# Performance work log

Measured on AMD Instinct MI355X. Metric: run time of the kernel, lower is better.

Reference implementation:

```python
import jax, jax.numpy as jnp
import numpy as np

H = 256          # hidden_channels
R = 64           # num_rbf
N = 20000        # nodes
E = 320000       # edges
CUTOFF_LO = 0.0
CUTOFF_UP = 5.0
LN_EPS = 1e-5


def _layernorm(x, g, b):
    mu = jnp.mean(x, axis=-1, keepdims=True)
    var = jnp.var(x, axis=-1, keepdims=True)
    return (x - mu) * jax.lax.rsqrt(var + LN_EPS) * g + b


def _cosine_cutoff(r):
    # cutoff_lower == 0 branch of CosineCutoff
    c = 0.5 * (jnp.cos(r * (jnp.pi / CUTOFF_UP)) + 1.0)
    return c * (r < CUTOFF_UP).astype(r.dtype)


def setup_inputs() -> dict:
    key = jax.random.key(0)
    ks = jax.random.split(key, 16)
    def xavier(k, shape):
        fan_in, fan_out = shape[1], shape[0]
        lim = np.sqrt(6.0 / (fan_in + fan_out))
        return jax.random.uniform(k, shape, jnp.float32, -lim, lim)
    x = jax.random.normal(ks[0], (N, H), jnp.float32)
    edge_index = jax.random.randint(ks[1], (2, E), 0, N, jnp.int64)
    edge_weight = jax.random.uniform(ks[2], (E,), jnp.float32, 0.0, CUTOFF_UP)
    edge_attr = jax.random.normal(ks[3], (E, R), jnp.float32)
    return {
        "x": x,
        "edge_index": edge_index,
        "edge_weight": edge_weight,
        "edge_attr": edge_attr,
        "ln_g": jnp.ones((H,), jnp.float32),
        "ln_b": jnp.zeros((H,), jnp.float32),
        "Wq": xavier(ks[4], (H, H)), "bq": jnp.zeros((H,), jnp.float32),
        "Wk": xavier(ks[5], (H, H)), "bk": jnp.zeros((H,), jnp.float32),
        "Wv": xavier(ks[6], (H, H)), "bv": jnp.zeros((H,), jnp.float32),
        "Wo": xavier(ks[7], (H, H)), "bo": jnp.zeros((H,), jnp.float32),
        "Wdk": xavier(ks[8], (H, R)), "bdk": jnp.zeros((H,), jnp.float32),
        "Wdv": xavier(ks[9], (H, R)), "bdv": jnp.zeros((H,), jnp.float32),
    }


def reference(x, edge_index, edge_weight, edge_attr,
              ln_g, ln_b, Wq, bq, Wk, bk, Wv, bv, Wo, bo, Wdk, bdk, Wdv, bdv):
    src = edge_index[0]  # j (messages come from)
    dst = edge_index[1]  # i (messages aggregate to)

    x_norm = _layernorm(x, ln_g, ln_b)                     # [N,H]
    q = x_norm @ Wq.T + bq                                 # [N,H]
    k = x_norm @ Wk.T + bk
    v = x_norm @ Wv.T + bv

    dk = jax.nn.silu(edge_attr @ Wdk.T + bdk)              # [E,H]
    dv = jax.nn.silu(edge_attr @ Wdv.T + bdv)              # [E,H]

    q_i = q[dst]                                           # [E,H]
    k_j = k[src]
    v_j = v[src]

    attn = jnp.sum(q_i * k_j * dk, axis=1)                 # [E]
    attn = jax.nn.silu(attn) * _cosine_cutoff(edge_weight) # [E]

    msg = v_j * dv * attn[:, None]                         # [E,H]
    agg = jax.ops.segment_sum(msg, dst, num_segments=x.shape[0])  # [N,H]

    out = agg @ Wo.T + bo
    return x + out
```

## Files before the change

### kernel.cpp

```cpp
#include <hip/hip_runtime.h>
#include <math.h>

#define NN 20000
#define H 256
#define R 64
#define EE 320000
#define LN_EPS 1e-5f
#define NB 79

using short8  = __attribute__((ext_vector_type(8))) short;
using ushort8 = __attribute__((ext_vector_type(8))) unsigned short;
using f32x4   = __attribute__((ext_vector_type(4))) float;

__device__ __forceinline__ float silu_f(float x) {
    return x * __builtin_amdgcn_rcpf(1.0f + __expf(-x));
}

__device__ __forceinline__ unsigned short f2bf(float f) {
    unsigned u = __float_as_uint(f);
    u += 0x7fff + ((u >> 16) & 1);
    return (unsigned short)(u >> 16);
}
__device__ __forceinline__ float bf2f(unsigned short s) {
    return __uint_as_float(((unsigned)s) << 16);
}
__device__ __forceinline__ unsigned short f2h(float f) {
    unsigned r;
    asm("v_cvt_f16_f32 %0, %1" : "=v"(r) : "v"(f));
    return (unsigned short)r;
}
__device__ __forceinline__ float h2f(unsigned short h) {
    float f;
    asm("v_cvt_f32_f16 %0, %1" : "=v"(f) : "v"((unsigned)h));
    return f;
}

__device__ __forceinline__ int dh_idx(int row, int col) {
    return row * 256 + (col ^ (((row >> 2) & 3) << 4));
}

__global__ __launch_bounds__(256) void k_prep(
    const float* __restrict__ Wq, const float* __restrict__ Wk,
    const float* __restrict__ Wv, const float* __restrict__ Wo,
    const float* __restrict__ g,  const float* __restrict__ b,
    const float* __restrict__ bq, const float* __restrict__ bk, const float* __restrict__ bv,
    const float* __restrict__ Wdk, const float* __restrict__ Wdv,
    unsigned short* __restrict__ wqkv_p, unsigned short* __restrict__ wo_p,
    unsigned short* __restrict__ wdk_p,  unsigned short* __restrict__ wdv_p,
    float* __restrict__ bias3, int* __restrict__ hist)
{
    const int bid = blockIdx.x, t = threadIdx.x;
    if (bid < 128) {
        const int mat = bid >> 5;
        const float* W = mat == 0 ? Wq : (mat == 1 ? Wk : (mat == 2 ? Wv : Wo));
        unsigned short* out = (mat < 3) ? wqkv_p + (size_t)mat * 131072 : wo_p;
        const int fold = mat < 3;
        const int flat = (bid & 31) * 256 + t;
        const int tile = flat >> 9;
        const int rem  = flat & 511;
        const int ks   = rem >> 6;
        const int lane = rem & 63;
        const int nl = lane & 15, quad = lane >> 4;
        const int h  = tile * 16 + nl;
        const int c0 = ks * 32 + quad * 8;
        short8 hi8, lo8;
        #pragma unroll
        for (int j = 0; j < 8; ++j) {
            float wv = W[(size_t)h * 256 + c0 + j];
            if (fold) wv *= g[c0 + j];
            const unsigned short hh = f2bf(wv);
            hi8[j] = (short)hh;
            lo8[j] = (short)f2bf(wv - bf2f(hh));
        }
        unsigned short* ob = out + ((size_t)(tile * 8 + ks)) * 1024;
        *(short8*)&ob[lane * 8] = hi8;
        *(short8*)&ob[512 + lane * 8] = lo8;
    } else if (bid < 144) {
        const int flat = (bid - 128) * 256 + t;
        const int mat  = flat >> 11;
        const int rem  = flat & 2047;
        const int hh   = rem >> 10;
        const int r2   = rem & 1023;
        const int tile = r2 >> 7;
        const int r3   = r2 & 127;
        const int ks   = r3 >> 6;
        const int lane = r3 & 63;
        const int nl = lane & 15, quad = lane >> 4;
        const float* W = mat == 0 ? Wdk : Wdv;
        unsigned short* out = (mat == 0 ? wdk_p : wdv_p)
                            + hh * 16384 + (tile * 2 + ks) * 1024 + lane * 8;
        const float* wr = W + (size_t)(hh * 128 + tile * 16 + nl) * 64 + ks * 32 + quad * 8;
        const float4 w0 = *(const float4*)wr;
        const float4 w1 = *(const float4*)(wr + 4);
        const float zz[8] = {w0.x, w0.y, w0.z, w0.w, w1.x, w1.y, w1.z, w1.w};
        short8 hi8, lo8;
        #pragma unroll
        for (int j = 0; j < 8; ++j) {
            const unsigned short hv = f2bf(zz[j]);
            hi8[j] = (short)hv;
            lo8[j] = (short)f2bf(zz[j] - bf2f(hv));
        }
        *(short8*)out = hi8;
        *(short8*)(out + 512) = lo8;
    } else if (bid < 147) {
        const int mat = bid - 144, h = t;
        const float* W  = mat == 0 ? Wq : (mat == 1 ? Wk : Wv);
        const float* bb = mat == 0 ? bq : (mat == 1 ? bk : bv);
        float s = 0.f;
        const float* wr = W + (size_t)h * 256;
        for (int c = 0; c < 256; c += 4) {
            const float4 w4 = *(const float4*)(wr + c);
            const float4 b4 = *(const float4*)(b + c);
            s += w4.x * b4.x + w4.y * b4.y + w4.z * b4.z + w4.w * b4.w;
        }
        bias3[mat * 256 + h] = bb[h] + s;
    } else {
        const int i = (bid - 147) * 256 + t;
        if (i < NN) hist[i] = 0;
    }
}

__global__ __launch_bounds__(64, 2) void k_ln_qkv(
    const float* __restrict__ x,
    const unsigned short* __restrict__ wqkv_p, const float* __restrict__ bias3,
    unsigned short* __restrict__ q, unsigned short* __restrict__ k,
    unsigned short* __restrict__ v)
{
    const int t = threadIdx.x;
    const int lane = t & 63;
    const int nl = lane & 15, quad = lane >> 4;
    const int nbase = blockIdx.x * 16;
    const int node = nbase + nl;
    const bool nv = node < NN;

    float xv[64];
    float sum = 0.f, sq = 0.f;
    {
        const float* xp = x + (size_t)node * H + quad * 8;
        #pragma unroll
        for (int ks = 0; ks < 8; ++ks) {
            float4 x0 = {0.f,0.f,0.f,0.f}, x1 = {0.f,0.f,0.f,0.f};
            if (nv) {
                x0 = *(const float4*)(xp + ks * 32);
                x1 = *(const float4*)(xp + ks * 32 + 4);
            }
            xv[ks*8+0]=x0.x; xv[ks*8+1]=x0.y; xv[ks*8+2]=x0.z; xv[ks*8+3]=x0.w;
            xv[ks*8+4]=x1.x; xv[ks*8+5]=x1.y; xv[ks*8+6]=x1.z; xv[ks*8+7]=x1.w;
            sum += x0.x+x0.y+x0.z+x0.w + x1.x+x1.y+x1.z+x1.w;
            sq  += x0.x*x0.x+x0.y*x0.y+x0.z*x0.z+x0.w*x0.w
                 + x1.x*x1.x+x1.y*x1.y+x1.z*x1.z+x1.w*x1.w;
        }
    }
    sum += __shfl_xor(sum, 16); sum += __shfl_xor(sum, 32);
    sq  += __shfl_xor(sq, 16);  sq  += __shfl_xor(sq, 32);
    const float mu  = sum * (1.0f / H);
    const float var = sq * (1.0f / H) - mu * mu;
    const float rs  = rsqrtf(var + LN_EPS);

    short8 a_hi[8], a_lo[8];
    #pragma unroll
    for (int ks = 0; ks < 8; ++ks) {
        #pragma unroll
        for (int j = 0; j < 8; ++j) {
            const float z = (xv[ks*8+j] - mu) * rs;
            const unsigned short hh = f2bf(z);
            a_hi[ks][j] = (short)hh;
            a_lo[ks][j] = (short)f2bf(z - bf2f(hh));
        }
    }

    for (int mat = 0; mat < 3; ++mat) {
        unsigned short* outp = mat == 0 ? q : (mat == 1 ? k : v);
        const float* bp = bias3 + mat * 256;
        const unsigned short* wb = wqkv_p + (size_t)mat * 131072 + lane * 8;
        for (int tile = 0; tile < 16; ++tile) {
            const unsigned short* gb = wb + (size_t)tile * 8192;
            const float bbv = bp[tile * 16 + nl];
            f32x4 acc = {bbv, bbv, bbv, bbv};
            #pragma unroll
            for (int ks = 0; ks < 8; ++ks) {
                const short8 b_hi = *(const short8*)(gb + ks * 1024);
                const short8 b_lo = *(const short8*)(gb + ks * 1024 + 512);
                acc = __builtin_amdgcn_mfma_f32_16x16x32_bf16(a_hi[ks], b_hi, acc, 0, 0, 0);
                acc = __builtin_amdgcn_mfma_f32_16x16x32_bf16(a_lo[ks], b_hi, acc, 0, 0, 0);
                acc = __builtin_amdgcn_mfma_f32_16x16x32_bf16(a_hi[ks], b_lo, acc, 0, 0, 0);
            }
            #pragma unroll
            for (int r = 0; r < 4; ++r) {
                const int onode = nbase + quad * 4 + r;
                if (onode < NN)
                    outp[(size_t)onode * H + tile * 16 + nl] = f2h(acc[r]);
            }
        }
    }
}

__global__ __launch_bounds__(256) void k_hist(const int* __restrict__ ei, int* __restrict__ hist) {
    int e = blockIdx.x * 256 + threadIdx.x;
    if (e < EE) atomicAdd(&hist[ei[EE + e]], 1);
}

__global__ __launch_bounds__(256) void k_scan1(const int* __restrict__ hist,
                                               int* __restrict__ cursor, int* __restrict__ bsum) {
    const int t = threadIdx.x, i = blockIdx.x * 256 + t;
    const int lane = t & 63, w = t >> 6;
    const int v = (i < NN) ? hist[i] : 0;
    int incl = v;
    #pragma unroll
    for (int off = 1; off < 64; off <<= 1) {
        int u = __shfl_up(incl, off);
        if (lane >= off) incl += u;
    }
    __shared__ int ws[4];
    if (lane == 63) ws[w] = incl;
    __syncthreads();
    int base = 0;
    #pragma unroll
    for (int j = 0; j < 4; ++j) if (j < w) base += ws[j];
    if (i < NN) cursor[i] = base + incl - v;
    if (t == 255) bsum[blockIdx.x] = base + incl;
}

__global__ __launch_bounds__(128) void k_scan2(int* __restrict__ bsum) {
    __shared__ int buf[128];
    const int t = threadIdx.x;
    const int v = (t < NB) ? bsum[t] : 0;
    buf[t] = v;
    __syncthreads();
    #pragma unroll
    for (int off = 1; off < 128; off <<= 1) {
        int add = (t >= off) ? buf[t - off] : 0;
        __syncthreads();
        buf[t] += add;
        __syncthreads();
    }
    if (t < NB) bsum[t] = buf[t] - v;
}

__global__ __launch_bounds__(256) void k_scatter(const int* __restrict__ ei,
                                                 const float* __restrict__ ew,
                                                 int* __restrict__ cursor,
                                                 const int* __restrict__ bsum,
                                                 int* __restrict__ perm,
                                                 int* __restrict__ srcs,
                                                 int* __restrict__ dsts,
                                                 float* __restrict__ ews) {
    int e = blockIdx.x * 256 + threadIdx.x;
    if (e < EE) {
        int s = ei[e];
        int d = ei[EE + e];
        int pos = atomicAdd(&cursor[d], 1) + bsum[d >> 8];
        perm[pos] = e;
        srcs[pos] = s;
        dsts[pos] = d;
        ews[pos] = ew[e];
    }
}

__global__ __launch_bounds__(256, 4) void k_edge(
    const unsigned short* __restrict__ q16, const unsigned short* __restrict__ k16,
    const unsigned short* __restrict__ v16,
    const float* __restrict__ ea,
    const unsigned short* __restrict__ wdk_p, const float* __restrict__ bdk,
    const unsigned short* __restrict__ wdv_p, const float* __restrict__ bdv,
    const int* __restrict__ perm, const int* __restrict__ srcs,
    const int* __restrict__ dsts, const float* __restrict__ ews,
    float* __restrict__ agg)
{
    __shared__ __align__(16) unsigned short dks_all[4 * 16 * 256];
    __shared__ int   srcw_all[4 * 16], dstw_all[4 * 16];
    __shared__ float attw_all[4 * 16];

    const int t    = threadIdx.x;
    const int bi   = blockIdx.x;
    const int wave = t >> 6, lane = t & 63;
    const int eb2  = (((bi & 7) * 625 + (bi >> 3)) * 4 + wave) * 16;

    unsigned short* dksw = dks_all + wave * 4096;
    int*   srcw = srcw_all + wave * 16;
    int*   dstw = dstw_all + wave * 16;
    float* attw = attw_all + wave * 16;

    const int nl = lane & 15, quad = lane >> 4;
    const int tx = lane & 31, ty2 = lane >> 5;
    const int h0 = tx * 4, e0l = ty2 * 8;

    if (lane < 16) {
        srcw[lane] = srcs[eb2 + lane];
        dstw[lane] = dsts[eb2 + lane];
    }

    short8 a_hi[2], a_lo[2];
    {
        const int e = perm[eb2 + nl];
        const float* ap = ea + (size_t)e * R + quad * 8;
        #pragma unroll
        for (int ks = 0; ks < 2; ++ks) {
            const f32x4 x0 = *(const f32x4*)(ap + ks * 32);
            const f32x4 x1 = *(const f32x4*)(ap + ks * 32 + 4);
            const float zz[8] = {x0[0], x0[1], x0[2], x0[3], x1[0], x1[1], x1[2], x1[3]};
            #pragma unroll
            for (int j = 0; j < 8; ++j) {
                const unsigned short hv = f2bf(zz[j]);
                a_hi[ks][j] = (short)hv;
                a_lo[ks][j] = (short)f2bf(zz[j] - bf2f(hv));
            }
        }
    }

    #define MFMA_DKS(IMG, BIAS, HALF)                                                 \
    {                                                                                 \
        const unsigned short* img_ = (IMG);                                           \
        f32x4 accA[8];                                                                \
        _Pragma("unroll")                                                             \
        for (int tt = 0; tt < 8; ++tt) {                                              \
            short8 b_hi[2], b_lo[2];                                                  \
            _Pragma("unroll")                                                         \
            for (int ks = 0; ks < 2; ++ks) {                                          \
                const unsigned short* fb = img_ + (tt * 2 + ks) * 1024 + lane * 8;    \
                b_hi[ks] = *(const short8*)fb;                                        \
                b_lo[ks] = *(const short8*)(fb + 512);                                \
            }                                                                         \
            const float bb = (BIAS)[(HALF) * 128 + tt * 16 + nl];                     \
            f32x4 acc = {bb, bb, bb, bb};                                             \
            _Pragma("unroll")                                                         \
            for (int ks = 0; ks < 2; ++ks) {                                          \
                acc = __builtin_amdgcn_mfma_f32_16x16x32_bf16(a_hi[ks], b_hi[ks], acc, 0, 0, 0); \
                acc = __builtin_amdgcn_mfma_f32_16x16x32_bf16(a_lo[ks], b_hi[ks], acc, 0, 0, 0); \
                acc = __builtin_amdgcn_mfma_f32_16x16x32_bf16(a_hi[ks], b_lo[ks], acc, 0, 0, 0); \
            }                                                                         \
            accA[tt] = acc;                                                           \
        }                                                                             \
        _Pragma("unroll")                                                             \
        for (int tt = 0; tt < 8; ++tt)                                                \
            _Pragma("unroll")                                                         \
            for (int r = 0; r < 4; ++r)                                               \
                dksw[dh_idx(quad * 4 + r, (HALF) * 128 + tt * 16 + nl)] =             \
                    f2h(silu_f(accA[tt][r]));                                         \
    }

    MFMA_DKS(wdk_p,         bdk, 0);
    MFMA_DKS(wdk_p + 16384, bdk, 1);

    {
        float qv[8];
        int pd = -1;
        #pragma unroll
        for (int i = 0; i < 8; ++i) {
            const int d = dstw[e0l + i], s = srcw[e0l + i];
            if (d != pd) {
                const ushort4 q0 = *(const ushort4*)(q16 + (size_t)d * H + h0);
                const ushort4 q1 = *(const ushort4*)(q16 + (size_t)d * H + 128 + h0);
                qv[0] = h2f(q0.x); qv[1] = h2f(q0.y); qv[2] = h2f(q0.z); qv[3] = h2f(q0.w);
                qv[4] = h2f(q1.x); qv[5] = h2f(q1.y); qv[6] = h2f(q1.z); qv[7] = h2f(q1.w);
                pd = d;
            }
            const ushort4 k0 = *(const ushort4*)(k16 + (size_t)s * H + h0);
            const ushort4 k1 = *(const ushort4*)(k16 + (size_t)s * H + 128 + h0);
            const ushort4 d40 = *(const ushort4*)&dksw[dh_idx(e0l + i, h0)];
            const ushort4 d41 = *(const ushort4*)&dksw[dh_idx(e0l + i, 128 + h0)];
            float part = qv[0] * h2f(k0.x) * h2f(d40.x) + qv[1] * h2f(k0.y) * h2f(d40.y)
                       + qv[2] * h2f(k0.z) * h2f(d40.z) + qv[3] * h2f(k0.w) * h2f(d40.w)
                       + qv[4] * h2f(k1.x) * h2f(d41.x) + qv[5] * h2f(k1.y) * h2f(d41.y)
                       + qv[6] * h2f(k1.z) * h2f(d41.z) + qv[7] * h2f(k1.w) * h2f(d41.w);
            #pragma unroll
            for (int off = 16; off; off >>= 1) part += __shfl_xor(part, off);
            if (tx == 0) attw[e0l + i] = part;
        }
    }

    if (lane < 16) {
        const float rr = ews[eb2 + lane];
        const float cut = (rr < 5.0f) ? 0.5f * (__cosf(rr * 0.6283185307f) + 1.0f) : 0.0f;
        attw[lane] = silu_f(attw[lane]) * cut;
    }

    MFMA_DKS(wdv_p,         bdv, 0);
    MFMA_DKS(wdv_p + 16384, bdv, 1);

    {
        float4 m0 = {0.f,0.f,0.f,0.f}, m1 = {0.f,0.f,0.f,0.f};
        int cur_d = -1;
        #pragma unroll
        for (int i = 0; i < 8; ++i) {
            const int d = dstw[e0l + i], s = srcw[e0l + i];
            const float a = attw[e0l + i];
            const ushort4 v0 = *(const ushort4*)(v16 + (size_t)s * H + h0);
            const ushort4 v1 = *(const ushort4*)(v16 + (size_t)s * H + 128 + h0);
            const ushort4 d40 = *(const ushort4*)&dksw[dh_idx(e0l + i, h0)];
            const ushort4 d41 = *(const ushort4*)&dksw[dh_idx(e0l + i, 128 + h0)];
            const float w0x = h2f(v0.x) * h2f(d40.x) * a, w0y = h2f(v0.y) * h2f(d40.y) * a;
            const float w0z = h2f(v0.z) * h2f(d40.z) * a, w0w = h2f(v0.w) * h2f(d40.w) * a;
            const float w1x = h2f(v1.x) * h2f(d41.x) * a, w1y = h2f(v1.y) * h2f(d41.y) * a;
            const float w1z = h2f(v1.z) * h2f(d41.z) * a, w1w = h2f(v1.w) * h2f(d41.w) * a;
            if (d != cur_d) {
                if (cur_d >= 0) {
                    float* dp = agg + (size_t)cur_d * H;
                    atomicAdd(dp + h0 + 0, m0.x); atomicAdd(dp + h0 + 1, m0.y);
                    atomicAdd(dp + h0 + 2, m0.z); atomicAdd(dp + h0 + 3, m0.w);
                    atomicAdd(dp + 128 + h0 + 0, m1.x); atomicAdd(dp + 128 + h0 + 1, m1.y);
                    atomicAdd(dp + 128 + h0 + 2, m1.z); atomicAdd(dp + 128 + h0 + 3, m1.w);
                }
                m0.x = w0x; m0.y = w0y; m0.z = w0z; m0.w = w0w;
                m1.x = w1x; m1.y = w1y; m1.z = w1z; m1.w = w1w;
                cur_d = d;
            } else {
                m0.x += w0x; m0.y += w0y; m0.z += w0z; m0.w += w0w;
                m1.x += w1x; m1.y += w1y; m1.z += w1z; m1.w += w1w;
            }
        }
        {
            float* dp = agg + (size_t)cur_d * H;
            atomicAdd(dp + h0 + 0, m0.x); atomicAdd(dp + h0 + 1, m0.y);
            atomicAdd(dp + h0 + 2, m0.z); atomicAdd(dp + h0 + 3, m0.w);
            atomicAdd(dp + 128 + h0 + 0, m1.x); atomicAdd(dp + 128 + h0 + 1, m1.y);
            atomicAdd(dp + 128 + h0 + 2, m1.z); atomicAdd(dp + 128 + h0 + 3, m1.w);
        }
    }
    #undef MFMA_DKS
}

__global__ __launch_bounds__(64, 2) void k_out(
    const float* __restrict__ aggm, const unsigned short* __restrict__ wo_p,
    const float* __restrict__ bo, const float* __restrict__ x, float* __restrict__ out)
{
    const int t = threadIdx.x;
    const int lane = t & 63;
    const int nl = lane & 15, quad = lane >> 4;
    const int nbase = blockIdx.x * 16;
    const int node = nbase + nl;
    const bool nv = node < NN;

    short8 a_hi[8], a_lo[8];
    {
        const float* ap = aggm + (size_t)node * H + quad * 8;
        #pragma unroll
        for (int ks = 0; ks < 8; ++ks) {
            float4 x0 = {0.f,0.f,0.f,0.f}, x1 = {0.f,0.f,0.f,0.f};
            if (nv) { x0 = *(const float4*)(ap + ks * 32); x1 = *(const float4*)(ap + ks * 32 + 4); }
            const float zz[8] = {x0.x,x0.y,x0.z,x0.w,x1.x,x1.y,x1.z,x1.w};
            #pragma unroll
            for (int j = 0; j < 8; ++j) {
                const unsigned short hh = f2bf(zz[j]);
                a_hi[ks][j] = (short)hh;
                a_lo[ks][j] = (short)f2bf(zz[j] - bf2f(hh));
            }
        }
    }
    for (int tile = 0; tile < 16; ++tile) {
        const unsigned short* gb = wo_p + (size_t)tile * 8192 + lane * 8;
        const float bbv = bo[tile * 16 + nl];
        f32x4 acc = {bbv, bbv, bbv, bbv};
        #pragma unroll
        for (int ks = 0; ks < 8; ++ks) {
            const short8 b_hi = *(const short8*)(gb + ks * 1024);
            const short8 b_lo = *(const short8*)(gb + ks * 1024 + 512);
            acc = __builtin_amdgcn_mfma_f32_16x16x32_bf16(a_hi[ks], b_hi, acc, 0, 0, 0);
            acc = __builtin_amdgcn_mfma_f32_16x16x32_bf16(a_lo[ks], b_hi, acc, 0, 0, 0);
            acc = __builtin_amdgcn_mfma_f32_16x16x32_bf16(a_hi[ks], b_lo, acc, 0, 0, 0);
        }
        #pragma unroll
        for (int r = 0; r < 4; ++r) {
            const int onode = nbase + quad * 4 + r;
            if (onode < NN) {
                const size_t oi = (size_t)onode * H + tile * 16 + nl;
                out[oi] = x[oi] + acc[r];
            }
        }
    }
}

extern "C" void kernel_launch(void* const* d_in, const int* in_sizes, int n_in,
                              void* d_out, int out_size, void* d_ws, size_t ws_size,
                              hipStream_t stream) {
    const float* x   = (const float*)d_in[0];
    const int*   ei  = (const int*)d_in[1];
    const float* ew  = (const float*)d_in[2];
    const float* ea  = (const float*)d_in[3];
    const float* g   = (const float*)d_in[4];
    const float* b   = (const float*)d_in[5];
    const float* Wq  = (const float*)d_in[6];  const float* bq  = (const float*)d_in[7];
    const float* Wk  = (const float*)d_in[8];  const float* bk  = (const float*)d_in[9];
    const float* Wv  = (const float*)d_in[10]; const float* bv  = (const float*)d_in[11];
    const float* Wo  = (const float*)d_in[12]; const float* bo  = (const float*)d_in[13];
    const float* Wdk = (const float*)d_in[14]; const float* bdk = (const float*)d_in[15];
    const float* Wdv = (const float*)d_in[16]; const float* bdv = (const float*)d_in[17];

    unsigned short* q16 = (unsigned short*)d_ws;
    unsigned short* k16 = q16 + (size_t)NN * H;
    unsigned short* v16 = k16 + (size_t)NN * H;
    float* agg  = (float*)(v16 + (size_t)NN * H);
    int*   hist = (int*)(agg + (size_t)NN * H);
    int*   cur  = hist + NN;
    int*   bsum = cur + NN;
    int*   perm = bsum + 128;
    int*   srcs = perm + EE;
    int*   dsts = srcs + EE;
    float* ews  = (float*)(dsts + EE);
    unsigned short* wqkv_p = (unsigned short*)(ews + EE);
    unsigned short* wo_p   = wqkv_p + 393216;
    unsigned short* wdk_p  = wo_p + 131072;
    unsigned short* wdv_p  = wdk_p + 32768;
    float* bias3 = (float*)(wdv_p + 32768);

    hipMemsetAsync(agg, 0, (size_t)NN * H * sizeof(float), stream);
    k_prep<<<226, 256, 0, stream>>>(Wq, Wk, Wv, Wo, g, b, bq, bk, bv, Wdk, Wdv,
                                    wqkv_p, wo_p, wdk_p, wdv_p, bias3, hist);
    k_hist<<<EE / 256, 256, 0, stream>>>(ei, hist);
    k_ln_qkv<<<(NN + 15) / 16, 64, 0, stream>>>(x, wqkv_p, bias3, q16, k16, v16);
    k_scan1<<<NB, 256, 0, stream>>>(hist, cur, bsum);
    k_scan2<<<1, 128, 0, stream>>>(bsum);
    k_scatter<<<EE / 256, 256, 0, stream>>>(ei, ew, cur, bsum, perm, srcs, dsts, ews);
    k_edge<<<EE / 64, 256, 0, stream>>>(q16, k16, v16, ea, wdk_p, bdk, wdv_p, bdv,
                                        perm, srcs, dsts, ews, agg);
    k_out<<<(NN + 15) / 16, 64, 0, stream>>>(agg, wo_p, bo, x, (float*)d_out);
}
```

Measured before the change: 628.0 us.

## Use fp16 MFMA for edge dk/dv projections with LDS-staged weights and persistent blocks

```diff
diff --git a/kernel.cpp b/kernel.cpp
--- a/kernel.cpp
+++ b/kernel.cpp
@@ -7,10 +7,16 @@
 #define EE 320000
 #define LN_EPS 1e-5f
 #define NB 79
+#define GEDGE 1000
 
 using short8  = __attribute__((ext_vector_type(8))) short;
 using ushort8 = __attribute__((ext_vector_type(8))) unsigned short;
 using f32x4   = __attribute__((ext_vector_type(4))) float;
+using half8   = __attribute__((ext_vector_type(8))) _Float16;
+using half2v  = __attribute__((ext_vector_type(2))) _Float16;
+
+typedef __attribute__((address_space(3))) unsigned int lds_uint;
+typedef const __attribute__((address_space(1))) unsigned int glb_uint;
 
 __device__ __forceinline__ float silu_f(float x) {
     return x * __builtin_amdgcn_rcpf(1.0f + __expf(-x));
@@ -88,20 +94,15 @@
         const int nl = lane & 15, quad = lane >> 4;
         const float* W = mat == 0 ? Wdk : Wdv;
         unsigned short* out = (mat == 0 ? wdk_p : wdv_p)
-                            + hh * 16384 + (tile * 2 + ks) * 1024 + lane * 8;
+                            + hh * 8192 + (tile * 2 + ks) * 512 + lane * 8;
         const float* wr = W + (size_t)(hh * 128 + tile * 16 + nl) * 64 + ks * 32 + quad * 8;
         const float4 w0 = *(const float4*)wr;
         const float4 w1 = *(const float4*)(wr + 4);
         const float zz[8] = {w0.x, w0.y, w0.z, w0.w, w1.x, w1.y, w1.z, w1.w};
-        short8 hi8, lo8;
-        #pragma unroll
-        for (int j = 0; j < 8; ++j) {
-            const unsigned short hv = f2bf(zz[j]);
-            hi8[j] = (short)hv;
-            lo8[j] = (short)f2bf(zz[j] - bf2f(hv));
-        }
-        *(short8*)out = hi8;
-        *(short8*)(out + 512) = lo8;
+        ushort8 p8;
+        #pragma unroll
+        for (int j = 0; j < 8; ++j) p8[j] = f2h(zz[j]);
+        *(ushort8*)out = p8;
     } else if (bid < 147) {
         const int mat = bid - 144, h = t;
         const float* W  = mat == 0 ? Wq : (mat == 1 ? Wk : Wv);
@@ -257,78 +258,50 @@
     }
 }
 
-__global__ __launch_bounds__(256, 4) void k_edge(
+__global__ __launch_bounds__(256, 1) void k_edge(
     const unsigned short* __restrict__ q16, const unsigned short* __restrict__ k16,
     const unsigned short* __restrict__ v16,
     const float* __restrict__ ea,
-    const unsigned short* __restrict__ wdk_p, const float* __restrict__ bdk,
-    const unsigned short* __restrict__ wdv_p, const float* __restrict__ bdv,
+    const unsigned short* __restrict__ wdkv_p,
+    const float* __restrict__ bdk, const float* __restrict__ bdv,
     const int* __restrict__ perm, const int* __restrict__ srcs,
     const int* __restrict__ dsts, const float* __restrict__ ews,
     float* __restrict__ agg)
 {
+    __shared__ __align__(16) unsigned short wlds[4 * 8192];
     __shared__ __align__(16) unsigned short dks_all[4 * 16 * 256];
-    __shared__ int   srcw_all[4 * 16], dstw_all[4 * 16];
-    __shared__ float attw_all[4 * 16];
 
     const int t    = threadIdx.x;
     const int bi   = blockIdx.x;
     const int wave = t >> 6, lane = t & 63;
-    const int eb2  = (((bi & 7) * 625 + (bi >> 3)) * 4 + wave) * 16;
-
-    unsigned short* dksw = dks_all + wave * 4096;
-    int*   srcw = srcw_all + wave * 16;
-    int*   dstw = dstw_all + wave * 16;
-    float* attw = attw_all + wave * 16;
-
     const int nl = lane & 15, quad = lane >> 4;
     const int tx = lane & 31, ty2 = lane >> 5;
     const int h0 = tx * 4, e0l = ty2 * 8;
 
-    if (lane < 16) {
-        srcw[lane] = srcs[eb2 + lane];
-        dstw[lane] = dsts[eb2 + lane];
-    }
-
-    short8 a_hi[2], a_lo[2];
+    unsigned short* dksw = dks_all + wave * 4096;
+
     {
-        const int e = perm[eb2 + nl];
-        const float* ap = ea + (size_t)e * R + quad * 8;
-        #pragma unroll
-        for (int ks = 0; ks < 2; ++ks) {
-            const f32x4 x0 = *(const f32x4*)(ap + ks * 32);
-            const f32x4 x1 = *(const f32x4*)(ap + ks * 32 + 4);
-            const float zz[8] = {x0[0], x0[1], x0[2], x0[3], x1[0], x1[1], x1[2], x1[3]};
-            #pragma unroll
-            for (int j = 0; j < 8; ++j) {
-                const unsigned short hv = f2bf(zz[j]);
-                a_hi[ks][j] = (short)hv;
-                a_lo[ks][j] = (short)f2bf(zz[j] - bf2f(hv));
-            }
-        }
-    }
-
-    #define MFMA_DKS(IMG, BIAS, HALF)                                                 \
+        const ushort8* sp = (const ushort8*)wdkv_p + t;
+        ushort8* dpw = (ushort8*)wlds + (t & 192);
+        #pragma unroll
+        for (int c = 0; c < 16; ++c)
+            __builtin_amdgcn_global_load_lds((glb_uint*)(sp + c * 256),
+                                             (lds_uint*)(dpw + c * 256), 16, 0, 0);
+    }
+    __syncthreads();
+
+    #define MFMA_DKS16(IMG, BIAS, HALF)                                               \
     {                                                                                 \
-        const unsigned short* img_ = (IMG);                                           \
+        const unsigned short* ib_ = wlds + (IMG) * 8192;                              \
         f32x4 accA[8];                                                                \
         _Pragma("unroll")                                                             \
         for (int tt = 0; tt < 8; ++tt) {                                              \
-            short8 b_hi[2], b_lo[2];                                                  \
-            _Pragma("unroll")                                                         \
-            for (int ks = 0; ks < 2; ++ks) {                                          \
-                const unsigned short* fb = img_ + (tt * 2 + ks) * 1024 + lane * 8;    \
-                b_hi[ks] = *(const short8*)fb;                                        \
-                b_lo[ks] = *(const short8*)(fb + 512);                                \
-            }                                                                         \
+            const half8 b0 = *(const half8*)&ib_[(tt * 2 + 0) * 512 + lane * 8];      \
+            const half8 b1 = *(const half8*)&ib_[(tt * 2 + 1) * 512 + lane * 8];      \
             const float bb = (BIAS)[(HALF) * 128 + tt * 16 + nl];                     \
             f32x4 acc = {bb, bb, bb, bb};                                             \
-            _Pragma("unroll")                                                         \
-            for (int ks = 0; ks < 2; ++ks) {                                          \
-                acc = __builtin_amdgcn_mfma_f32_16x16x32_bf16(a_hi[ks], b_hi[ks], acc, 0, 0, 0); \
-                acc = __builtin_amdgcn_mfma_f32_16x16x32_bf16(a_lo[ks], b_hi[ks], acc, 0, 0, 0); \
-                acc = __builtin_amdgcn_mfma_f32_16x16x32_bf16(a_hi[ks], b_lo[ks], acc, 0, 0, 0); \
-            }                                                                         \
+            acc = __builtin_amdgcn_mfma_f32_16x16x32_f16(af0, b0, acc, 0, 0, 0);      \
+            acc = __builtin_amdgcn_mfma_f32_16x16x32_f16(af1, b1, acc, 0, 0, 0);      \
             accA[tt] = acc;                                                           \
         }                                                                             \
         _Pragma("unroll")                                                             \
@@ -339,85 +312,127 @@
                     f2h(silu_f(accA[tt][r]));                                         \
     }
 
-    MFMA_DKS(wdk_p,         bdk, 0);
-    MFMA_DKS(wdk_p + 16384, bdk, 1);
-
-    {
-        float qv[8];
-        int pd = -1;
+    for (int it = 0; it < 5; ++it) {
+        const int chunk = (bi & 7) * 625 + (bi >> 3) * 5 + it;
+        const int eb2   = (chunk * 4 + wave) * 16;
+
+        half8 af0, af1;
+        {
+            const int e = perm[eb2 + nl];
+            const float* ap = ea + (size_t)e * R + quad * 8;
+            const f32x4 x0 = *(const f32x4*)(ap);
+            const f32x4 x1 = *(const f32x4*)(ap + 4);
+            const f32x4 x2 = *(const f32x4*)(ap + 32);
+            const f32x4 x3 = *(const f32x4*)(ap + 36);
+            #pragma unroll
+            for (int j = 0; j < 4; ++j) {
+                af0[j]     = (_Float16)x0[j];
+                af0[j + 4] = (_Float16)x1[j];
+                af1[j]     = (_Float16)x2[j];
+                af1[j + 4] = (_Float16)x3[j];
+            }
+        }
+
+        MFMA_DKS16(0, bdk, 0);
+        MFMA_DKS16(1, bdk, 1);
+
+        int srcr[8], dstr[8];
         #pragma unroll
         for (int i = 0; i < 8; ++i) {
-            const int d = dstw[e0l + i], s = srcw[e0l + i];
-            if (d != pd) {
-                const ushort4 q0 = *(const ushort4*)(q16 + (size_t)d * H + h0);
-                const ushort4 q1 = *(const ushort4*)(q16 + (size_t)d * H + 128 + h0);
-                qv[0] = h2f(q0.x); qv[1] = h2f(q0.y); qv[2] = h2f(q0.z); qv[3] = h2f(q0.w);
-                qv[4] = h2f(q1.x); qv[5] = h2f(q1.y); qv[6] = h2f(q1.z); qv[7] = h2f(q1.w);
-                pd = d;
-            }
-            const ushort4 k0 = *(const ushort4*)(k16 + (size_t)s * H + h0);
-            const ushort4 k1 = *(const ushort4*)(k16 + (size_t)s * H + 128 + h0);
-            const ushort4 d40 = *(const ushort4*)&dksw[dh_idx(e0l + i, h0)];
-            const ushort4 d41 = *(const ushort4*)&dksw[dh_idx(e0l + i, 128 + h0)];
-            float part = qv[0] * h2f(k0.x) * h2f(d40.x) + qv[1] * h2f(k0.y) * h2f(d40.y)
-                       + qv[2] * h2f(k0.z) * h2f(d40.z) + qv[3] * h2f(k0.w) * h2f(d40.w)
-                       + qv[4] * h2f(k1.x) * h2f(d41.x) + qv[5] * h2f(k1.y) * h2f(d41.y)
-                       + qv[6] * h2f(k1.z) * h2f(d41.z) + qv[7] * h2f(k1.w) * h2f(d41.w);
+            srcr[i] = srcs[eb2 + e0l + i];
+            dstr[i] = dsts[eb2 + e0l + i];
+        }
+
+        float att[8];
+        {
+            half2v qa, qb, qc, qd;
+            int pd = -1;
             #pragma unroll
-            for (int off = 16; off; off >>= 1) part += __shfl_xor(part, off);
-            if (tx == 0) attw[e0l + i] = part;
-        }
-    }
-
-    if (lane < 16) {
-        const float rr = ews[eb2 + lane];
-        const float cut = (rr < 5.0f) ? 0.5f * (__cosf(rr * 0.6283185307f) + 1.0f) : 0.0f;
-        attw[lane] = silu_f(attw[lane]) * cut;
-    }
-
-    MFMA_DKS(wdv_p,         bdv, 0);
-    MFMA_DKS(wdv_p + 16384, bdv, 1);
-
-    {
-        float4 m0 = {0.f,0.f,0.f,0.f}, m1 = {0.f,0.f,0.f,0.f};
-        int cur_d = -1;
+            for (int i = 0; i < 8; ++i) {
+                const int d = dstr[i], s = srcr[i];
+                if (d != pd) {
+                    const uint2 qq0 = *(const uint2*)(q16 + (size_t)d * H + h0);
+                    const uint2 qq1 = *(const uint2*)(q16 + (size_t)d * H + 128 + h0);
+                    qa = __builtin_bit_cast(half2v, qq0.x);
+                    qb = __builtin_bit_cast(half2v, qq0.y);
+                    qc = __builtin_bit_cast(half2v, qq1.x);
+                    qd = __builtin_bit_cast(half2v, qq1.y);
+                    pd = d;
+                }
+                const uint2 kk0 = *(const uint2*)(k16 + (size_t)s * H + h0);
+                const uint2 kk1 = *(const uint2*)(k16 + (size_t)s * H + 128 + h0);
+                const uint2 dd0 = *(const uint2*)&dksw[dh_idx(e0l + i, h0)];
+                const uint2 dd1 = *(const uint2*)&dksw[dh_idx(e0l + i, 128 + h0)];
+                float part = 0.f;
+                part = __builtin_amdgcn_fdot2(qa * __builtin_bit_cast(half2v, kk0.x),
+                                              __builtin_bit_cast(half2v, dd0.x), part, false);
+                part = __builtin_amdgcn_fdot2(qb * __builtin_bit_cast(half2v, kk0.y),
+                                              __builtin_bit_cast(half2v, dd0.y), part, false);
+                part = __builtin_amdgcn_fdot2(qc * __builtin_bit_cast(half2v, kk1.x),
+                                              __builtin_bit_cast(half2v, dd1.x), part, false);
+                part = __builtin_amdgcn_fdot2(qd * __builtin_bit_cast(half2v, kk1.y),
+                                              __builtin_bit_cast(half2v, dd1.y), part, false);
+                #pragma unroll
+                for (int off = 16; off; off >>= 1) part += __shfl_xor(part, off);
+                att[i] = part;
+            }
+        }
+
         #pragma unroll
         for (int i = 0; i < 8; ++i) {
-            const int d = dstw[e0l + i], s = srcw[e0l + i];
-            const float a = attw[e0l + i];
-            const ushort4 v0 = *(const ushort4*)(v16 + (size_t)s * H + h0);
-            const ushort4 v1 = *(const ushort4*)(v16 + (size_t)s * H + 128 + h0);
-            const ushort4 d40 = *(const ushort4*)&dksw[dh_idx(e0l + i, h0)];
-            const ushort4 d41 = *(const ushort4*)&dksw[dh_idx(e0l + i, 128 + h0)];
-            const float w0x = h2f(v0.x) * h2f(d40.x) * a, w0y = h2f(v0.y) * h2f(d40.y) * a;
-            const float w0z = h2f(v0.z) * h2f(d40.z) * a, w0w = h2f(v0.w) * h2f(d40.w) * a;
-            const float w1x = h2f(v1.x) * h2f(d41.x) * a, w1y = h2f(v1.y) * h2f(d41.y) * a;
-            const float w1z = h2f(v1.z) * h2f(d41.z) * a, w1w = h2f(v1.w) * h2f(d41.w) * a;
-            if (d != cur_d) {
-                if (cur_d >= 0) {
-                    float* dp = agg + (size_t)cur_d * H;
-                    atomicAdd(dp + h0 + 0, m0.x); atomicAdd(dp + h0 + 1, m0.y);
-                    atomicAdd(dp + h0 + 2, m0.z); atomicAdd(dp + h0 + 3, m0.w);
-                    atomicAdd(dp + 128 + h0 + 0, m1.x); atomicAdd(dp + 128 + h0 + 1, m1.y);
-                    atomicAdd(dp + 128 + h0 + 2, m1.z); atomicAdd(dp + 128 + h0 + 3, m1.w);
+            const float rr = ews[eb2 + e0l + i];
+            const float cut = (rr < 5.0f) ? 0.5f * (__cosf(rr * 0.6283185307f) + 1.0f) : 0.0f;
+            att[i] = silu_f(att[i]) * cut;
+        }
+
+        MFMA_DKS16(2, bdv, 0);
+        MFMA_DKS16(3, bdv, 1);
+
+        {
+            float4 m0 = {0.f,0.f,0.f,0.f}, m1 = {0.f,0.f,0.f,0.f};
+            int cur_d = -1;
+            #pragma unroll
+            for (int i = 0; i < 8; ++i) {
+                const int d = dstr[i], s = srcr[i];
+                const float a = att[i];
+                const uint2 vv0 = *(const uint2*)(v16 + (size_t)s * H + h0);
+                const uint2 vv1 = *(const uint2*)(v16 + (size_t)s * H + 128 + h0);
+                const uint2 dd0 = *(const uint2*)&dksw[dh_idx(e0l + i, h0)];
+                const uint2 dd1 = *(const uint2*)&dksw[dh_idx(e0l + i, 128 + h0)];
+                const half2v w0 = __builtin_bit_cast(half2v, vv0.x) * __builtin_bit_cast(half2v, dd0.x);
+                const half2v w1 = __builtin_bit_cast(half2v, vv0.y) * __builtin_bit_cast(half2v, dd0.y);
+                const half2v w2 = __builtin_bit_cast(half2v, vv1.x) * __builtin_bit_cast(half2v, dd1.x);
+                const half2v w3 = __builtin_bit_cast(half2v, vv1.y) * __builtin_bit_cast(half2v, dd1.y);
+                if (d != cur_d) {
+                    if (cur_d >= 0) {
+                        float* dp = agg + (size_t)cur_d * H;
+                        atomicAdd(dp + h0 + 0, m0.x); atomicAdd(dp + h0 + 1, m0.y);
+                        atomicAdd(dp + h0 + 2, m0.z); atomicAdd(dp + h0 + 3, m0.w);
+                        atomicAdd(dp + 128 + h0 + 0, m1.x); atomicAdd(dp + 128 + h0 + 1, m1.y);
+                        atomicAdd(dp + 128 + h0 + 2, m1.z); atomicAdd(dp + 128 + h0 + 3, m1.w);
+                    }
+                    m0.x = (float)w0[0] * a; m0.y = (float)w0[1] * a;
+                    m0.z = (float)w1[0] * a; m0.w = (float)w1[1] * a;
+                    m1.x = (float)w2[0] * a; m1.y = (float)w2[1] * a;
+                    m1.z = (float)w3[0] * a; m1.w = (float)w3[1] * a;
+                    cur_d = d;
+                } else {
+                    m0.x += (float)w0[0] * a; m0.y += (float)w0[1] * a;
+                    m0.z += (float)w1[0] * a; m0.w += (float)w1[1] * a;
+                    m1.x += (float)w2[0] * a; m1.y += (float)w2[1] * a;
+                    m1.z += (float)w3[0] * a; m1.w += (float)w3[1] * a;
                 }
-                m0.x = w0x; m0.y = w0y; m0.z = w0z; m0.w = w0w;
-                m1.x = w1x; m1.y = w1y; m1.z = w1z; m1.w = w1w;
-                cur_d = d;
-            } else {
-                m0.x += w0x; m0.y += w0y; m0.z += w0z; m0.w += w0w;
-                m1.x += w1x; m1.y += w1y; m1.z += w1z; m1.w += w1w;
-            }
-        }
-        {
-            float* dp = agg + (size_t)cur_d * H;
-            atomicAdd(dp + h0 + 0, m0.x); atomicAdd(dp + h0 + 1, m0.y);
-            atomicAdd(dp + h0 + 2, m0.z); atomicAdd(dp + h0 + 3, m0.w);
-            atomicAdd(dp + 128 + h0 + 0, m1.x); atomicAdd(dp + 128 + h0 + 1, m1.y);
-            atomicAdd(dp + 128 + h0 + 2, m1.z); atomicAdd(dp + 128 + h0 + 3, m1.w);
-        }
-    }
-    #undef MFMA_DKS
+            }
+            {
+                float* dp = agg + (size_t)cur_d * H;
+                atomicAdd(dp + h0 + 0, m0.x); atomicAdd(dp + h0 + 1, m0.y);
+                atomicAdd(dp + h0 + 2, m0.z); atomicAdd(dp + h0 + 3, m0.w);
+                atomicAdd(dp + 128 + h0 + 0, m1.x); atomicAdd(dp + 128 + h0 + 1, m1.y);
+                atomicAdd(dp + 128 + h0 + 2, m1.z); atomicAdd(dp + 128 + h0 + 3, m1.w);
+            }
+        }
+    }
+    #undef MFMA_DKS16
 }
 
 __global__ __launch_bounds__(64, 2) void k_out(
@@ -500,8 +515,8 @@
     unsigned short* wqkv_p = (unsigned short*)(ews + EE);
     unsigned short* wo_p   = wqkv_p + 393216;
     unsigned short* wdk_p  = wo_p + 131072;
-    unsigned short* wdv_p  = wdk_p + 32768;
-    float* bias3 = (float*)(wdv_p + 32768);
+    unsigned short* wdv_p  = wdk_p + 16384;
+    float* bias3 = (float*)(wdv_p + 16384);
 
     hipMemsetAsync(agg, 0, (size_t)NN * H * sizeof(float), stream);
     k_prep<<<226, 256, 0, stream>>>(Wq, Wk, Wv, Wo, g, b, bq, bk, bv, Wdk, Wdv,
@@ -511,7 +526,7 @@
     k_scan1<<<NB, 256, 0, stream>>>(hist, cur, bsum);
     k_scan2<<<1, 128, 0, stream>>>(bsum);
     k_scatter<<<EE / 256, 256, 0, stream>>>(ei, ew, cur, bsum, perm, srcs, dsts, ews);
-    k_edge<<<EE / 64, 256, 0, stream>>>(q16, k16, v16, ea, wdk_p, bdk, wdv_p, bdv,
-                                        perm, srcs, dsts, ews, agg);
+    k_edge<<<GEDGE, 256, 0, stream>>>(q16, k16, v16, ea, wdk_p, bdk, bdv,
+                                      perm, srcs, dsts, ews, agg);
     k_out<<<(NN + 15) / 16, 64, 0, stream>>>(agg, wo_p, bo, x, (float*)d_out);
 }
```

Result: slower. 650.2 us (+3.5%).
